# Performance work log

Measured on AMD Instinct MI355X. Metric: run time of the kernel, lower is better.

## Reference

```python
import jax, jax.numpy as jnp
import numpy as np

N_NODES = 10000
N_EDGES = 160000
N_REL = 4
N_GRAPHS = 256
IN_DIM = 64


def rgcn_layer(x, W, root, bias, src, dst, etype, num_nodes, num_rel):
    # PyG RGCNConv with default aggr='mean': per-relation mean aggregation,
    # plus root transform and bias.
    h = jnp.einsum('nd,rdf->rnf', x, W)            # [R, N, F] grouped GEMM
    msg = h[etype, src]                             # [E, F] gather per edge
    comb = dst * num_rel + etype                    # (dst, relation) bucket
    cnt = jax.ops.segment_sum(jnp.ones(etype.shape, x.dtype), comb,
                              num_segments=num_nodes * num_rel)
    inv = 1.0 / jnp.maximum(cnt, 1.0)
    msg = msg * inv[comb][:, None]                  # per-relation mean norm
    agg = jax.ops.segment_sum(msg, dst, num_segments=num_nodes)  # scatter-add
    return agg + x @ root + bias


def global_mean_pool(x, batch, num_graphs):
    s = jax.ops.segment_sum(x, batch, num_segments=num_graphs)
    c = jax.ops.segment_sum(jnp.ones(batch.shape, x.dtype), batch,
                            num_segments=num_graphs)
    return s / jnp.maximum(c, 1.0)[:, None]


def setup_inputs() -> dict:
    key = jax.random.key(0)
    ks = jax.random.split(key, 20)
    s = 0.02
    inp = {
        'x': jax.random.normal(ks[0], (N_NODES, IN_DIM), jnp.float32),
        'edge_index': jax.random.randint(ks[1], (2, N_EDGES), 0, N_NODES),
        'edge_type': jax.random.randint(ks[2], (N_EDGES,), 0, N_REL),
        'batch': jnp.sort(jax.random.randint(ks[3], (N_NODES,), 0, N_GRAPHS)),
        'W1': jax.random.normal(ks[4], (N_REL, IN_DIM, 1024), jnp.float32) * s,
        'root1': jax.random.normal(ks[5], (IN_DIM, 1024), jnp.float32) * s,
        'b1': jnp.zeros((1024,), jnp.float32),
        'W2': jax.random.normal(ks[6], (N_REL, 1024, 1024), jnp.float32) * s,
        'root2': jax.random.normal(ks[7], (1024, 1024), jnp.float32) * s,
        'b2': jnp.zeros((1024,), jnp.float32),
        'W3': jax.random.normal(ks[8], (N_REL, 1024, 712), jnp.float32) * s,
        'root3': jax.random.normal(ks[9], (1024, 712), jnp.float32) * s,
        'b3': jnp.zeros((712,), jnp.float32),
        'fw1': jax.random.normal(ks[10], (712, 64), jnp.float32) * s,
        'fb1': jnp.zeros((64,), jnp.float32),
        'fw2': jax.random.normal(ks[11], (64, 1), jnp.float32) * s,
        'fb2': jnp.zeros((1,), jnp.float32),
    }
    return inp


def reference(x, edge_index, edge_type, batch, W1, root1, b1, W2, root2, b2,
              W3, root3, b3, fw1, fb1, fw2, fb2):
    src, dst = edge_index[0], edge_index[1]
    # dropout is a no-op in eval mode (training=False)
    h = jax.nn.relu(rgcn_layer(x, W1, root1, b1, src, dst, edge_type, N_NODES, N_REL))
    h = jax.nn.relu(rgcn_layer(h, W2, root2, b2, src, dst, edge_type, N_NODES, N_REL))
    h = jax.nn.relu(rgcn_layer(h, W3, root3, b3, src, dst, edge_type, N_NODES, N_REL))
    g = global_mean_pool(h, batch, N_GRAPHS)        # [G, 712]
    g = jax.nn.relu(g @ fw1 + fb1)
    out = g @ fw2 + fb2                             # [G, 1]
    return out
```

## Files before the change

### kernel.cpp

```cpp
#include <hip/hip_runtime.h>
#include <stdint.h>

#define N_NODES 10000
#define N_EDGES 160000
#define N_REL   4
#define N_GRAPHS 256
#define NBUCKET (N_NODES * N_REL)

typedef __attribute__((ext_vector_type(8))) short short8;
typedef __attribute__((ext_vector_type(4))) float float4v;

__device__ __forceinline__ unsigned short f2bf(float f) {
  unsigned int u = __float_as_uint(f);
  u = u + 0x7FFFu + ((u >> 16) & 1u);
  return (unsigned short)(u >> 16);
}
__device__ __forceinline__ float bf2f(unsigned short b) {
  return __uint_as_float(((unsigned int)b) << 16);
}

__device__ __forceinline__ void g2lds16(const void* g, void* l) {
  __builtin_amdgcn_global_load_lds(
      (const __attribute__((address_space(1))) void*)g,
      (__attribute__((address_space(3))) void*)l, 16, 0, 0);
}

__device__ __forceinline__ int lower_bound_i(const int* a, int n, int key) {
  int lo = 0, hi = n;
  while (lo < hi) { int mid = (lo + hi) >> 1; if (a[mid] < key) lo = mid + 1; else hi = mid; }
  return lo;
}

__global__ void count_edges_k(const int* __restrict__ ei, const int* __restrict__ et,
                              int* __restrict__ cnt, int E) {
  int e = blockIdx.x * 256 + threadIdx.x;
  if (e < E) atomicAdd(&cnt[ei[E + e] * N_REL + et[e]], 1);
}

__global__ void scan_block_k(const int* __restrict__ cnt, int* __restrict__ eexcl,
                             int* __restrict__ btot, int n) {
  int i = blockIdx.x * 256 + threadIdx.x;
  int v = (i < n) ? cnt[i] : 0;
  int lane = threadIdx.x & 63, wv = threadIdx.x >> 6;
  int s = v;
  #pragma unroll
  for (int off = 1; off < 64; off <<= 1) {
    int t = __shfl_up(s, off, 64);
    if (lane >= off) s += t;
  }
  __shared__ int wt[4];
  if (lane == 63) wt[wv] = s;
  __syncthreads();
  int wadd = 0;
  for (int w = 0; w < wv; ++w) wadd += wt[w];
  int incl = s + wadd;
  if (i < n) eexcl[i] = incl - v;
  if (threadIdx.x == 255) btot[blockIdx.x] = incl;
}

__global__ void scan_final_k(const int* __restrict__ cnt, const int* __restrict__ eexcl,
                             const int* __restrict__ btot, int* __restrict__ offs,
                             int* __restrict__ cursor, float* __restrict__ inv, int n) {
  __shared__ int wred[4];
  __shared__ int sboff;
  int t = threadIdx.x;
  int part = (t < (int)blockIdx.x) ? btot[t] : 0;
  #pragma unroll
  for (int off = 32; off > 0; off >>= 1) part += __shfl_down(part, off, 64);
  if ((t & 63) == 0) wred[t >> 6] = part;
  __syncthreads();
  if (t == 0) sboff = wred[0] + wred[1] + wred[2] + wred[3];
  __syncthreads();
  int i = blockIdx.x * 256 + t;
  if (i < n) {
    int o = sboff + eexcl[i];
    offs[i] = o;
    cursor[i] = o;
    int c = cnt[i];
    inv[i] = 1.0f / (float)(c > 1 ? c : 1);
  }
}

__global__ void fill_csr_k(const int* __restrict__ ei, const int* __restrict__ et,
                           int* __restrict__ cursor, int* __restrict__ elist, int E) {
  int e = blockIdx.x * 256 + threadIdx.x;
  if (e >= E) return;
  int dst = ei[E + e], src = ei[e], r = et[e];
  int pos = atomicAdd(&cursor[dst * N_REL + r], 1);
  elist[pos] = src;
}

__device__ __forceinline__ void wcat_body(const float* __restrict__ W,
                                          const float* __restrict__ root,
                                          unsigned short* __restrict__ out,
                                          int Din4, int F, int K,
                                          int bx, int by, int tx, int ty,
                                          float (*tile)[33]) {
  int kb = bx * 32, fb = by * 32;
  for (int i = ty; i < 32; i += 8) {
    int k = kb + i, f = fb + tx;
    float v = 0.0f;
    if (k < K && f < F) v = (k < Din4) ? W[(size_t)k * F + f] : root[(size_t)(k - Din4) * F + f];
    tile[i][tx] = v;
  }
  __syncthreads();
  for (int i = ty; i < 32; i += 8) {
    int f = fb + i, k = kb + tx;
    if (f < F && k < K) out[(size_t)f * K + k] = f2bf(tile[tx][i]);
  }
}

__global__ __launch_bounds__(256) void agg64_wcat_k(
    const float* __restrict__ x, const int* __restrict__ offs,
    const int* __restrict__ cnt, const float* __restrict__ inv,
    const int* __restrict__ elist, unsigned short* __restrict__ Xcat,
    const float* __restrict__ W, const float* __restrict__ root,
    unsigned short* __restrict__ WcatT, int wcatGX) {
  __shared__ float tile[32][33];
  if (blockIdx.x < N_NODES) {
    const int n = blockIdx.x;
    const int wv = threadIdx.x >> 6;
    const int col = threadIdx.x & 63;
    const int b = n * N_REL + wv;
    const int start = offs[b], c = cnt[b];
    const float sc = inv[b];
    float acc = 0.0f;
    int j = 0;
    for (; j + 2 <= c; j += 2) {
      int s0 = elist[start + j], s1 = elist[start + j + 1];
      float v0 = x[(size_t)s0 * 64 + col];
      float v1 = x[(size_t)s1 * 64 + col];
      acc += v0; acc += v1;
    }
    for (; j < c; ++j) {
      int s = elist[start + j];
      acc += x[(size_t)s * 64 + col];
    }
    Xcat[(size_t)n * 320 + wv * 64 + col] = f2bf(acc * sc);
    if (wv == 0)
      Xcat[(size_t)n * 320 + 256 + col] = f2bf(x[(size_t)n * 64 + col]);
  } else {
    int bb = blockIdx.x - N_NODES;
    int bx = bb % wcatGX, by = bb / wcatGX;
    wcat_body(W, root, WcatT, 256, 1024, 320, bx, by,
              threadIdx.x & 31, threadIdx.x >> 5, tile);
  }
}

__global__ __launch_bounds__(256) void aggbf16_wcat_k(
    const unsigned short* __restrict__ h,
    const int* __restrict__ offs, const int* __restrict__ cnt,
    const float* __restrict__ inv, const int* __restrict__ elist,
    unsigned short* __restrict__ Xcat,
    const float* __restrict__ W, const float* __restrict__ root,
    unsigned short* __restrict__ WcatT, int wcatGX, int Din4, int F, int K) {
  __shared__ float tile[32][33];
  if (blockIdx.x < N_NODES) {
    const int bid = blockIdx.x;
    const int chunk = (bid & 7) >> 1;
    const int wv = threadIdx.x >> 6;
    const int lane = threadIdx.x & 63;
    const int n = ((bid >> 3) << 3) | ((bid & 1) << 2) | wv;
    const int col = chunk * 256 + (lane << 2);
    const int Din = 1024, K5 = 5120;
    const int b0 = n * N_REL;

    #pragma unroll
    for (int r = 0; r < N_REL; ++r) {
      const int sr = offs[b0 + r];
      const int c = cnt[b0 + r];
      float a0 = 0.f, a1 = 0.f, a2 = 0.f, a3 = 0.f;
      int j = 0;
      for (; j + 4 <= c; j += 4) {
        const int s0 = elist[sr + j + 0];
        const int s1 = elist[sr + j + 1];
        const int s2 = elist[sr + j + 2];
        const int s3 = elist[sr + j + 3];
        ushort4 v0 = *(const ushort4*)(h + (size_t)s0 * Din + col);
        ushort4 v1 = *(const ushort4*)(h + (size_t)s1 * Din + col);
        ushort4 v2 = *(const ushort4*)(h + (size_t)s2 * Din + col);
        ushort4 v3 = *(const ushort4*)(h + (size_t)s3 * Din + col);
        a0 += bf2f(v0.x); a1 += bf2f(v0.y); a2 += bf2f(v0.z); a3 += bf2f(v0.w);
        a0 += bf2f(v1.x); a1 += bf2f(v1.y); a2 += bf2f(v1.z); a3 += bf2f(v1.w);
        a0 += bf2f(v2.x); a1 += bf2f(v2.y); a2 += bf2f(v2.z); a3 += bf2f(v2.w);
        a0 += bf2f(v3.x); a1 += bf2f(v3.y); a2 += bf2f(v3.z); a3 += bf2f(v3.w);
      }
      for (; j < c; ++j) {
        const int s = elist[sr + j];
        ushort4 v = *(const ushort4*)(h + (size_t)s * Din + col);
        a0 += bf2f(v.x); a1 += bf2f(v.y); a2 += bf2f(v.z); a3 += bf2f(v.w);
      }
      const float sc = inv[b0 + r];
      ushort4 o;
      o.x = f2bf(a0 * sc); o.y = f2bf(a1 * sc);
      o.z = f2bf(a2 * sc); o.w = f2bf(a3 * sc);
      *(ushort4*)&Xcat[(size_t)n * K5 + r * Din + col] = o;
    }
    *(ushort4*)&Xcat[(size_t)n * K5 + 4 * Din + col] =
        *(const ushort4*)(h + (size_t)n * Din + col);
  } else {
    int bb = blockIdx.x - N_NODES;
    int bx = bb % wcatGX, by = bb / wcatGX;
    wcat_body(W, root, WcatT, Din4, F, K, bx, by,
              threadIdx.x & 31, threadIdx.x >> 5, tile);
  }
}

__global__ __launch_bounds__(256) void gemm_bt_bias_relu_k(
    const short* __restrict__ A, const short* __restrict__ Bt,
    const float* __restrict__ bias, unsigned short* __restrict__ C,
    int M, int Ndim, int K, int NX) {
  __shared__ short As[128 * 64];
  __shared__ short Bs[128 * 64];

  const int bid = blockIdx.x;
  const int xcd = bid & 7;
  const int local = bid >> 3;
  const int t = xcd * (NX * 10) + local;
  const int tileM = t / NX;
  const int tileN = t - tileM * NX;
  const int mBase = tileM * 128;
  const int nBase = tileN * 128;

  const int tid = threadIdx.x;
  const int wave = tid >> 6;
  const int lane = tid & 63;
  const int half = lane >> 4;
  const int lrow = lane & 15;
  const int wm = (wave >> 1) * 64;
  const int wn = (wave & 1) * 64;
  const int srow = lane >> 3;
  const int schunk = (lane & 7) ^ srow;

  float4v acc[4][4] = {};

  for (int k0 = 0; k0 < K; k0 += 64) {
    #pragma unroll
    for (int p = 0; p < 4; ++p) {
      int rb = wave * 32 + p * 8;
      int r = rb + srow;
      int gr = mBase + r; if (gr > M - 1) gr = M - 1;
      g2lds16(A + (size_t)gr * K + k0 + schunk * 8, &As[rb * 64]);
      int gn = nBase + r; if (gn > Ndim - 1) gn = Ndim - 1;
      g2lds16(Bt + (size_t)gn * K + k0 + schunk * 8, &Bs[rb * 64]);
    }
    __syncthreads();

    #pragma unroll
    for (int kk = 0; kk < 2; ++kk) {
      short8 a[4], b[4];
      #pragma unroll
      for (int i = 0; i < 4; ++i) {
        int r = wm + i * 16 + lrow;
        int q = (kk * 4 + half) ^ (r & 7);
        a[i] = *(const short8*)&As[r * 64 + q * 8];
      }
      #pragma unroll
      for (int j = 0; j < 4; ++j) {
        int r = wn + j * 16 + lrow;
        int q = (kk * 4 + half) ^ (r & 7);
        b[j] = *(const short8*)&Bs[r * 64 + q * 8];
      }
      #pragma unroll
      for (int i = 0; i < 4; ++i)
        #pragma unroll
        for (int j = 0; j < 4; ++j)
          acc[i][j] = __builtin_amdgcn_mfma_f32_16x16x32_bf16(a[i], b[j], acc[i][j], 0, 0, 0);
    }
    __syncthreads();
  }

  #pragma unroll
  for (int i = 0; i < 4; ++i) {
    int row0 = mBase + wm + i * 16 + half * 4;
    #pragma unroll
    for (int j = 0; j < 4; ++j) {
      int col = nBase + wn + j * 16 + lrow;
      if (col < Ndim) {
        float bv = bias[col];
        #pragma unroll
        for (int r = 0; r < 4; ++r) {
          int rr = row0 + r;
          if (rr < M) C[(size_t)rr * Ndim + col] = f2bf(fmaxf(acc[i][j][r] + bv, 0.0f));
        }
      }
    }
  }
}

__global__ __launch_bounds__(256) void pool_mlp_k(
    const unsigned short* __restrict__ h, const int* __restrict__ batch,
    const float* __restrict__ fw1, const float* __restrict__ fb1,
    const float* __restrict__ fw2, const float* __restrict__ fb2,
    float* __restrict__ out, int N, int F) {
  __shared__ float gsh[712];
  __shared__ float part[4][64];

  const int gid = blockIdx.x;
  const int tid = threadIdx.x;
  const int lo = lower_bound_i(batch, N, gid);
  const int hi = lower_bound_i(batch, N, gid + 1);
  const float scale = (hi > lo) ? 1.0f / (float)(hi - lo) : 0.0f;
  const int C4 = F >> 2;

  if (tid < C4) {
    float a0 = 0.f, a1 = 0.f, a2 = 0.f, a3 = 0.f;
    for (int n = lo; n < hi; ++n) {
      ushort4 v = *(const ushort4*)(h + (size_t)n * F + tid * 4);
      a0 += bf2f(v.x); a1 += bf2f(v.y); a2 += bf2f(v.z); a3 += bf2f(v.w);
    }
    gsh[tid * 4 + 0] = a0 * scale;
    gsh[tid * 4 + 1] = a1 * scale;
    gsh[tid * 4 + 2] = a2 * scale;
    gsh[tid * 4 + 3] = a3 * scale;
  }
  __syncthreads();

  const int f = tid & 63;
  const int wv = tid >> 6;
  const int d0 = wv * 178;
  const int d1 = min(d0 + 178, F);
  float a = 0.0f;
  int d = d0;
  for (; d + 3 < d1; d += 4) {
    float g0 = gsh[d], g1 = gsh[d + 1], g2 = gsh[d + 2], g3 = gsh[d + 3];
    a += g0 * fw1[(size_t)d * 64 + f]
       + g1 * fw1[(size_t)(d + 1) * 64 + f]
       + g2 * fw1[(size_t)(d + 2) * 64 + f]
       + g3 * fw1[(size_t)(d + 3) * 64 + f];
  }
  for (; d < d1; ++d) a += gsh[d] * fw1[(size_t)d * 64 + f];
  part[wv][f] = a;
  __syncthreads();

  if (tid < 64) {
    float hsum = part[0][tid] + part[1][tid] + part[2][tid] + part[3][tid] + fb1[tid];
    hsum = fmaxf(hsum, 0.0f);
    float p = hsum * fw2[tid];
    #pragma unroll
    for (int off = 32; off > 0; off >>= 1) p += __shfl_down(p, off, 64);
    if (tid == 0) out[gid] = p + fb2[0];
  }
}

extern "C" void kernel_launch(void* const* d_in, const int* in_sizes, int n_in,
                              void* d_out, int out_size, void* d_ws, size_t ws_size,
                              hipStream_t stream) {
  (void)in_sizes; (void)n_in; (void)out_size;
  const float* x    = (const float*)d_in[0];
  const int*  ei    = (const int*)d_in[1];
  const int*  et    = (const int*)d_in[2];
  const int*  batch = (const int*)d_in[3];
  const float* W1 = (const float*)d_in[4],  *root1 = (const float*)d_in[5],  *b1 = (const float*)d_in[6];
  const float* W2 = (const float*)d_in[7],  *root2 = (const float*)d_in[8],  *b2 = (const float*)d_in[9];
  const float* W3 = (const float*)d_in[10], *root3 = (const float*)d_in[11], *b3 = (const float*)d_in[12];
  const float* fw1 = (const float*)d_in[13], *fb1 = (const float*)d_in[14];
  const float* fw2 = (const float*)d_in[15], *fb2 = (const float*)d_in[16];
  float* out = (float*)d_out;

  char* ws = (char*)d_ws;
  size_t off = 0;
  auto alloc = [&](size_t bytes) -> void* {
    void* p = ws + off; off += (bytes + 255) & ~(size_t)255; return p;
  };
  int*   cnt    = (int*)alloc(NBUCKET * 4);
  int*   offs   = (int*)alloc(NBUCKET * 4);
  int*   cursor = (int*)alloc(NBUCKET * 4);
  int*   eexcl  = (int*)alloc(NBUCKET * 4);
  int*   btot   = (int*)alloc(256 * 4);
  int*   elist  = (int*)alloc(N_EDGES * 4);
  float* inv    = (float*)alloc(NBUCKET * 4);
  unsigned short* Xcat  = (unsigned short*)alloc((size_t)N_NODES * 5120 * 2);
  unsigned short* WcatT = (unsigned short*)alloc((size_t)1024 * 5120 * 2);
  unsigned short* hA = (unsigned short*)alloc((size_t)N_NODES * 1024 * 2);
  unsigned short* hB = (unsigned short*)alloc((size_t)N_NODES * 1024 * 2);
  (void)ws_size;

  hipMemsetAsync(cnt, 0, NBUCKET * 4, stream);
  count_edges_k<<<(N_EDGES + 255) / 256, 256, 0, stream>>>(ei, et, cnt, N_EDGES);
  int nsb = (NBUCKET + 255) / 256;
  scan_block_k<<<nsb, 256, 0, stream>>>(cnt, eexcl, btot, NBUCKET);
  scan_final_k<<<nsb, 256, 0, stream>>>(cnt, eexcl, btot, offs, cursor, inv, NBUCKET);
  fill_csr_k<<<(N_EDGES + 255) / 256, 256, 0, stream>>>(ei, et, cursor, elist, N_EDGES);

  agg64_wcat_k<<<N_NODES + 10 * 32, 256, 0, stream>>>(
      x, offs, cnt, inv, elist, Xcat, W1, root1, WcatT, 10);
  gemm_bt_bias_relu_k<<<8 * 80, 256, 0, stream>>>(
      (const short*)Xcat, (const short*)WcatT, b1, hA, N_NODES, 1024, 320, 8);

  aggbf16_wcat_k<<<N_NODES + 160 * 32, 256, 0, stream>>>(
      hA, offs, cnt, inv, elist, Xcat, W2, root2, WcatT, 160, 4096, 1024, 5120);
  gemm_bt_bias_relu_k<<<8 * 80, 256, 0, stream>>>(
      (const short*)Xcat, (const short*)WcatT, b2, hB, N_NODES, 1024, 5120, 8);

  aggbf16_wcat_k<<<N_NODES + 160 * 23, 256, 0, stream>>>(
      hB, offs, cnt, inv, elist, Xcat, W3, root3, WcatT, 160, 4096, 712, 5120);
  gemm_bt_bias_relu_k<<<6 * 80, 256, 0, stream>>>(
      (const short*)Xcat, (const short*)WcatT, b3, hA, N_NODES, 712, 5120, 6);

  pool_mlp_k<<<N_GRAPHS, 256, 0, stream>>>(hA, batch, fw1, fb1, fw2, fb2, out,
                                           N_NODES, 712);
}
```

Baseline: 549.6 us.

## Read root features directly in GEMM and move weight packing into GEMM launches

```diff
diff --git a/kernel.cpp b/kernel.cpp
--- a/kernel.cpp
+++ b/kernel.cpp
@@ -147,71 +147,71 @@
   }
 }
 
-__global__ __launch_bounds__(256) void aggbf16_wcat_k(
+__global__ __launch_bounds__(256) void aggbf16_k(
     const unsigned short* __restrict__ h,
     const int* __restrict__ offs, const int* __restrict__ cnt,
     const float* __restrict__ inv, const int* __restrict__ elist,
-    unsigned short* __restrict__ Xcat,
-    const float* __restrict__ W, const float* __restrict__ root,
-    unsigned short* __restrict__ WcatT, int wcatGX, int Din4, int F, int K) {
-  __shared__ float tile[32][33];
-  if (blockIdx.x < N_NODES) {
-    const int bid = blockIdx.x;
-    const int chunk = (bid & 7) >> 1;
-    const int wv = threadIdx.x >> 6;
-    const int lane = threadIdx.x & 63;
-    const int n = ((bid >> 3) << 3) | ((bid & 1) << 2) | wv;
-    const int col = chunk * 256 + (lane << 2);
-    const int Din = 1024, K5 = 5120;
-    const int b0 = n * N_REL;
-
-    #pragma unroll
-    for (int r = 0; r < N_REL; ++r) {
-      const int sr = offs[b0 + r];
-      const int c = cnt[b0 + r];
-      float a0 = 0.f, a1 = 0.f, a2 = 0.f, a3 = 0.f;
-      int j = 0;
-      for (; j + 4 <= c; j += 4) {
-        const int s0 = elist[sr + j + 0];
-        const int s1 = elist[sr + j + 1];
-        const int s2 = elist[sr + j + 2];
-        const int s3 = elist[sr + j + 3];
-        ushort4 v0 = *(const ushort4*)(h + (size_t)s0 * Din + col);
-        ushort4 v1 = *(const ushort4*)(h + (size_t)s1 * Din + col);
-        ushort4 v2 = *(const ushort4*)(h + (size_t)s2 * Din + col);
-        ushort4 v3 = *(const ushort4*)(h + (size_t)s3 * Din + col);
-        a0 += bf2f(v0.x); a1 += bf2f(v0.y); a2 += bf2f(v0.z); a3 += bf2f(v0.w);
-        a0 += bf2f(v1.x); a1 += bf2f(v1.y); a2 += bf2f(v1.z); a3 += bf2f(v1.w);
-        a0 += bf2f(v2.x); a1 += bf2f(v2.y); a2 += bf2f(v2.z); a3 += bf2f(v2.w);
-        a0 += bf2f(v3.x); a1 += bf2f(v3.y); a2 += bf2f(v3.z); a3 += bf2f(v3.w);
-      }
-      for (; j < c; ++j) {
-        const int s = elist[sr + j];
-        ushort4 v = *(const ushort4*)(h + (size_t)s * Din + col);
-        a0 += bf2f(v.x); a1 += bf2f(v.y); a2 += bf2f(v.z); a3 += bf2f(v.w);
-      }
-      const float sc = inv[b0 + r];
-      ushort4 o;
-      o.x = f2bf(a0 * sc); o.y = f2bf(a1 * sc);
-      o.z = f2bf(a2 * sc); o.w = f2bf(a3 * sc);
-      *(ushort4*)&Xcat[(size_t)n * K5 + r * Din + col] = o;
-    }
-    *(ushort4*)&Xcat[(size_t)n * K5 + 4 * Din + col] =
-        *(const ushort4*)(h + (size_t)n * Din + col);
-  } else {
-    int bb = blockIdx.x - N_NODES;
-    int bx = bb % wcatGX, by = bb / wcatGX;
-    wcat_body(W, root, WcatT, Din4, F, K, bx, by,
-              threadIdx.x & 31, threadIdx.x >> 5, tile);
+    unsigned short* __restrict__ Xcat) {
+  const int bid = blockIdx.x;
+  const int chunk = (bid & 7) >> 1;
+  const int wv = threadIdx.x >> 6;
+  const int lane = threadIdx.x & 63;
+  const int n = ((bid >> 3) << 3) | ((bid & 1) << 2) | wv;
+  const int col = chunk * 256 + (lane << 2);
+  const int Din = 1024, KA = 4096;
+  const int b0 = n * N_REL;
+
+  #pragma unroll
+  for (int r = 0; r < N_REL; ++r) {
+    const int sr = offs[b0 + r];
+    const int c = cnt[b0 + r];
+    float a0 = 0.f, a1 = 0.f, a2 = 0.f, a3 = 0.f;
+    int j = 0;
+    for (; j + 4 <= c; j += 4) {
+      const int s0 = elist[sr + j + 0];
+      const int s1 = elist[sr + j + 1];
+      const int s2 = elist[sr + j + 2];
+      const int s3 = elist[sr + j + 3];
+      ushort4 v0 = *(const ushort4*)(h + (size_t)s0 * Din + col);
+      ushort4 v1 = *(const ushort4*)(h + (size_t)s1 * Din + col);
+      ushort4 v2 = *(const ushort4*)(h + (size_t)s2 * Din + col);
+      ushort4 v3 = *(const ushort4*)(h + (size_t)s3 * Din + col);
+      a0 += bf2f(v0.x); a1 += bf2f(v0.y); a2 += bf2f(v0.z); a3 += bf2f(v0.w);
+      a0 += bf2f(v1.x); a1 += bf2f(v1.y); a2 += bf2f(v1.z); a3 += bf2f(v1.w);
+      a0 += bf2f(v2.x); a1 += bf2f(v2.y); a2 += bf2f(v2.z); a3 += bf2f(v2.w);
+      a0 += bf2f(v3.x); a1 += bf2f(v3.y); a2 += bf2f(v3.z); a3 += bf2f(v3.w);
+    }
+    for (; j < c; ++j) {
+      const int s = elist[sr + j];
+      ushort4 v = *(const ushort4*)(h + (size_t)s * Din + col);
+      a0 += bf2f(v.x); a1 += bf2f(v.y); a2 += bf2f(v.z); a3 += bf2f(v.w);
+    }
+    const float sc = inv[b0 + r];
+    ushort4 o;
+    o.x = f2bf(a0 * sc); o.y = f2bf(a1 * sc);
+    o.z = f2bf(a2 * sc); o.w = f2bf(a3 * sc);
+    *(ushort4*)&Xcat[(size_t)n * KA + r * Din + col] = o;
   }
 }
 
 __global__ __launch_bounds__(256) void gemm_bt_bias_relu_k(
-    const short* __restrict__ A, const short* __restrict__ Bt,
+    const short* __restrict__ A, int KA,
+    const short* __restrict__ rootA, int aggK,
+    const short* __restrict__ Bt,
     const float* __restrict__ bias, unsigned short* __restrict__ C,
-    int M, int Ndim, int K, int NX) {
+    int M, int Ndim, int K, int NX, int gemmNB,
+    const float* __restrict__ wW, const float* __restrict__ wRoot,
+    unsigned short* __restrict__ wOut, int wGX, int wDin4, int wF, int wK) {
   __shared__ short As[128 * 64];
   __shared__ short Bs[128 * 64];
+
+  if ((int)blockIdx.x >= gemmNB) {
+    int bb = blockIdx.x - gemmNB;
+    float (*tile)[33] = (float (*)[33])As;
+    wcat_body(wW, wRoot, wOut, wDin4, wF, wK, bb % wGX, bb / wGX,
+              threadIdx.x & 31, threadIdx.x >> 5, tile);
+    return;
+  }
 
   const int bid = blockIdx.x;
   const int xcd = bid & 7;
@@ -240,7 +240,10 @@
       int rb = wave * 32 + p * 8;
       int r = rb + srow;
       int gr = mBase + r; if (gr > M - 1) gr = M - 1;
-      g2lds16(A + (size_t)gr * K + k0 + schunk * 8, &As[rb * 64]);
+      const short* aSrc;
+      if (k0 < aggK) aSrc = A + (size_t)gr * KA + k0;
+      else           aSrc = rootA + (size_t)gr * 1024 + (k0 - aggK);
+      g2lds16(aSrc + schunk * 8, &As[rb * 64]);
       int gn = nBase + r; if (gn > Ndim - 1) gn = Ndim - 1;
       g2lds16(Bt + (size_t)gn * K + k0 + schunk * 8, &Bs[rb * 64]);
     }
@@ -370,8 +373,9 @@
   int*   btot   = (int*)alloc(256 * 4);
   int*   elist  = (int*)alloc(N_EDGES * 4);
   float* inv    = (float*)alloc(NBUCKET * 4);
-  unsigned short* Xcat  = (unsigned short*)alloc((size_t)N_NODES * 5120 * 2);
-  unsigned short* WcatT = (unsigned short*)alloc((size_t)1024 * 5120 * 2);
+  unsigned short* Xcat  = (unsigned short*)alloc((size_t)N_NODES * 4096 * 2);
+  unsigned short* WcatA = (unsigned short*)alloc((size_t)1024 * 5120 * 2);
+  unsigned short* WcatB = (unsigned short*)alloc((size_t)1024 * 5120 * 2);
   unsigned short* hA = (unsigned short*)alloc((size_t)N_NODES * 1024 * 2);
   unsigned short* hB = (unsigned short*)alloc((size_t)N_NODES * 1024 * 2);
   (void)ws_size;
@@ -384,19 +388,23 @@
   fill_csr_k<<<(N_EDGES + 255) / 256, 256, 0, stream>>>(ei, et, cursor, elist, N_EDGES);
 
   agg64_wcat_k<<<N_NODES + 10 * 32, 256, 0, stream>>>(
-      x, offs, cnt, inv, elist, Xcat, W1, root1, WcatT, 10);
-  gemm_bt_bias_relu_k<<<8 * 80, 256, 0, stream>>>(
-      (const short*)Xcat, (const short*)WcatT, b1, hA, N_NODES, 1024, 320, 8);
-
-  aggbf16_wcat_k<<<N_NODES + 160 * 32, 256, 0, stream>>>(
-      hA, offs, cnt, inv, elist, Xcat, W2, root2, WcatT, 160, 4096, 1024, 5120);
-  gemm_bt_bias_relu_k<<<8 * 80, 256, 0, stream>>>(
-      (const short*)Xcat, (const short*)WcatT, b2, hB, N_NODES, 1024, 5120, 8);
-
-  aggbf16_wcat_k<<<N_NODES + 160 * 23, 256, 0, stream>>>(
-      hB, offs, cnt, inv, elist, Xcat, W3, root3, WcatT, 160, 4096, 712, 5120);
+      x, offs, cnt, inv, elist, Xcat, W1, root1, WcatA, 10);
+  gemm_bt_bias_relu_k<<<8 * 80 + 160 * 32, 256, 0, stream>>>(
+      (const short*)Xcat, 320, nullptr, 320,
+      (const short*)WcatA, b1, hA, N_NODES, 1024, 320, 8, 8 * 80,
+      W2, root2, WcatB, 160, 4096, 1024, 5120);
+
+  aggbf16_k<<<N_NODES, 256, 0, stream>>>(hA, offs, cnt, inv, elist, Xcat);
+  gemm_bt_bias_relu_k<<<8 * 80 + 160 * 23, 256, 0, stream>>>(
+      (const short*)Xcat, 4096, (const short*)hA, 4096,
+      (const short*)WcatB, b2, hB, N_NODES, 1024, 5120, 8, 8 * 80,
+      W3, root3, WcatA, 160, 4096, 712, 5120);
+
+  aggbf16_k<<<N_NODES, 256, 0, stream>>>(hB, offs, cnt, inv, elist, Xcat);
   gemm_bt_bias_relu_k<<<6 * 80, 256, 0, stream>>>(
-      (const short*)Xcat, (const short*)WcatT, b3, hA, N_NODES, 712, 5120, 6);
+      (const short*)Xcat, 4096, (const short*)hB, 4096,
+      (const short*)WcatA, b3, hA, N_NODES, 712, 5120, 6, 6 * 80,
+      nullptr, nullptr, nullptr, 1, 0, 0, 0);
 
   pool_mlp_k<<<N_GRAPHS, 256, 0, stream>>>(hA, batch, fw1, fb1, fw2, fb2, out,
                                            N_NODES, 712);
```

Measured after the change: 550.5 us (median of 2 runs). No clear change (+0.2%).
